# Kernel tuning notes

Hardware: AMD Instinct MI355X
Metric: run time of the kernel (lower is better)

The kernel has to match this reference:

```python
import jax, jax.numpy as jnp
import numpy as np

VOCAB, D, H = 30522, 768, 128
B, S = 32, 1024
N_SENT, SENT_LEN = 16, 64


def _lstm_dir(x, W_ih, W_hh, b, reverse=False):
    """Single-direction LSTM, PyTorch gate order (i,f,g,o). x: [B,T,D] -> [B,T,H]."""
    pre = jnp.einsum('btd,gd->btg', x, W_ih) + b  # [B,T,4H]
    if reverse:
        pre = pre[:, ::-1]
    nb = x.shape[0]
    h0 = jnp.zeros((nb, H), x.dtype)

    def step(carry, xt):
        h, c = carry
        g = xt + h @ W_hh.T
        i, f, gg, o = jnp.split(g, 4, axis=-1)
        c = jax.nn.sigmoid(f) * c + jax.nn.sigmoid(i) * jnp.tanh(gg)
        h = jax.nn.sigmoid(o) * jnp.tanh(c)
        return (h, c), h

    _, hs = jax.lax.scan(step, (h0, h0), jnp.swapaxes(pre, 0, 1))
    hs = jnp.swapaxes(hs, 0, 1)  # [B,T,H]
    if reverse:
        hs = hs[:, ::-1]
    return hs


def _bilstm(x, Wf, Uf, bf, Wb, Ub, bb):
    return jnp.concatenate([_lstm_dir(x, Wf, Uf, bf, False),
                            _lstm_dir(x, Wb, Ub, bb, True)], axis=-1)


def setup_inputs() -> dict:
    key = jax.random.key(0)
    ks = jax.random.split(key, 20)
    p = lambda i, shape: (jax.random.normal(ks[i], shape, dtype=jnp.float32) * 0.05)
    inp = {
        'word_inputs': jax.random.randint(ks[0], (B, S), 0, VOCAB, dtype=jnp.int32),
        'sent_tokens': jax.random.randint(ks[1], (B, N_SENT, SENT_LEN), 0, VOCAB, dtype=jnp.int32),
        'seq_len': S,
        'E': p(2, (VOCAB, D)),
        'lstm_Wih_f': p(3, (4 * H, D)), 'lstm_Whh_f': p(4, (4 * H, H)), 'lstm_b_f': p(5, (4 * H,)),
        'lstm_Wih_b': p(6, (4 * H, D)), 'lstm_Whh_b': p(7, (4 * H, H)), 'lstm_b_b': p(8, (4 * H,)),
        'sent_Wih_f': p(9, (4 * H, D)), 'sent_Whh_f': p(10, (4 * H, H)), 'sent_b_f': p(11, (4 * H,)),
        'sent_Wih_b': p(12, (4 * H, D)), 'sent_Whh_b': p(13, (4 * H, H)), 'sent_b_b': p(14, (4 * H,)),
        'gate_W': p(15, (2 * H, 4 * H)), 'gate_b': p(16, (2 * H,)),
    }
    return inp


def reference(word_inputs, sent_tokens, seq_len, E,
              lstm_Wih_f, lstm_Whh_f, lstm_b_f, lstm_Wih_b, lstm_Whh_b, lstm_b_b,
              sent_Wih_f, sent_Whh_f, sent_b_f, sent_Wih_b, sent_Whh_b, sent_b_b,
              gate_W, gate_b):
    # wordrep: embedding lookup (full-length sequences, all-ones masks)
    word_rep = E[word_inputs]  # [B,S,D]
    feature_out = _bilstm(word_rep, lstm_Wih_f, lstm_Whh_f, lstm_b_f,
                          lstm_Wih_b, lstm_Whh_b, lstm_b_b)  # [B,S,2H]

    # per-sentence BiLSTM: each sentence has its own fresh hidden state, so
    # the original python loop over sentences == batched BiLSTM over (B*N, L)
    st = sent_tokens.reshape(B * N_SENT, SENT_LEN)
    sent_rep = E[st]  # [B*N, L, D]
    sent_out = _bilstm(sent_rep, sent_Wih_f, sent_Whh_f, sent_b_f,
                       sent_Wih_b, sent_Whh_b, sent_b_b)  # [B*N, L, 2H]
    feature_out_sents = sent_out.reshape(B, N_SENT * SENT_LEN, 2 * H)  # [B,S,2H]

    gamma = jax.nn.sigmoid(
        jnp.concatenate([feature_out, feature_out_sents], axis=-1) @ gate_W.T + gate_b)
    return gamma * feature_out + (1.0 - gamma) * feature_out_sents
```

## Files before the change

### kernel.cpp

```cpp
#include <hip/hip_runtime.h>

typedef unsigned short u16;
typedef __attribute__((ext_vector_type(8))) short short8;
typedef __attribute__((ext_vector_type(4))) float f32x4;

__device__ __forceinline__ u16 f2b(float f){
    unsigned u = __builtin_bit_cast(unsigned, f);
    u += 0x7fffu + ((u >> 16) & 1u);
    return (u16)(u >> 16);
}
__device__ __forceinline__ float b2f(u16 s){
    unsigned u = ((unsigned)s) << 16;
    return __builtin_bit_cast(float, u);
}
__device__ __forceinline__ float sigm(float x){ return 1.f/(1.f + __expf(-x)); }
__device__ __forceinline__ float tanhf2(float x){
    float e = __expf(2.f * x);
    return 1.f - 2.f/(1.f + e);
}

__global__ __launch_bounds__(256) void cvt_bf16(const float* __restrict__ s,
                                                u16* __restrict__ d, int n4){
    int i = blockIdx.x*256 + threadIdx.x;
    if (i < n4){
        float4 v = ((const float4*)s)[i];
        ushort4 o;
        o.x = f2b(v.x); o.y = f2b(v.y); o.z = f2b(v.z); o.w = f2b(v.w);
        ((ushort4*)d)[i] = o;
    }
}

__global__ __launch_bounds__(192) void cvt_wih_perm(const float* __restrict__ s,
                                                    u16* __restrict__ d){
    int r = blockIdx.x;
    int j = threadIdx.x;
    int g = r >> 7, u = r & 127;
    int ro = u * 4 + g;
    float4 v = ((const float4*)(s + (size_t)r * 768))[j];
    ushort4 o;
    o.x = f2b(v.x); o.y = f2b(v.y); o.z = f2b(v.z); o.w = f2b(v.w);
    ((ushort4*)(d + (size_t)ro * 768))[j] = o;
}

__global__ __launch_bounds__(256) void cvt_whh_perm(const float* __restrict__ s,
                                                    u16* __restrict__ d){
    int idx = blockIdx.x*256 + threadIdx.x;
    if (idx >= 512*32) return;
    int r = idx >> 5, j = idx & 31;
    int g = r >> 7, u = r & 127;
    int ro = u * 4 + g;
    float4 v = ((const float4*)(s + (size_t)r * 128))[j];
    ushort4 o;
    o.x = f2b(v.x); o.y = f2b(v.y); o.z = f2b(v.z); o.w = f2b(v.w);
    ((ushort4*)(d + (size_t)ro * 128))[j] = o;
}

__global__ __launch_bounds__(256) void gemm_embed(
    const u16* __restrict__ E, const int* __restrict__ tok,
    const u16* __restrict__ Wt, const float* __restrict__ bf_,
    const float* __restrict__ bb_, u16* __restrict__ pre, int sentMode)
{
    __shared__ __align__(16) u16 Asm[128*32];
    __shared__ __align__(16) u16 Bsm[128*32];
    const int m0 = blockIdx.x * 128, n0 = blockIdx.y * 128;
    const int tid = threadIdx.x;
    const int ar = tid >> 2, ch = (tid & 3) * 8;
    const u16* ap0 = E + (size_t)tok[m0 + ar] * 768 + ch;
    const u16* ap1 = E + (size_t)tok[m0 + 64 + ar] * 768 + ch;
    const u16* bp0 = Wt + (size_t)(n0 + ar) * 768 + ch;
    const u16* bp1 = Wt + (size_t)(n0 + 64 + ar) * 768 + ch;
    const int lane = tid & 63, wave = tid >> 6;
    const int wm = (wave >> 1) * 64, wn = (wave & 1) * 64;
    const int qr = lane >> 4, lr = lane & 15;
    f32x4 acc[4][4] = {};
    for (int k0 = 0; k0 < 768; k0 += 32){
        __syncthreads();
        *(short8*)&Asm[ar*32 + ch]      = *(const short8*)(ap0 + k0);
        *(short8*)&Asm[(64+ar)*32 + ch] = *(const short8*)(ap1 + k0);
        *(short8*)&Bsm[ar*32 + ch]      = *(const short8*)(bp0 + k0);
        *(short8*)&Bsm[(64+ar)*32 + ch] = *(const short8*)(bp1 + k0);
        __syncthreads();
        short8 af[4], bfr[4];
        #pragma unroll
        for (int i = 0; i < 4; ++i){
            af[i]  = *(const short8*)&Asm[(wm + i*16 + lr)*32 + qr*8];
            bfr[i] = *(const short8*)&Bsm[(wn + i*16 + lr)*32 + qr*8];
        }
        #pragma unroll
        for (int i = 0; i < 4; ++i)
            #pragma unroll
            for (int j = 0; j < 4; ++j)
                acc[i][j] = __builtin_amdgcn_mfma_f32_16x16x32_bf16(af[i], bfr[j], acc[i][j], 0, 0, 0);
    }
    #pragma unroll
    for (int j = 0; j < 4; ++j){
        int col = n0 + wn + j*16 + lr;
        int dirO = col >> 9, pcol = col & 511;
        int uu = pcol >> 2, gg = pcol & 3;
        float bias = (dirO ? bb_ : bf_)[gg*128 + uu];
        int wL = uu >> 4, uL = uu & 15;
        #pragma unroll
        for (int i = 0; i < 4; ++i){
            #pragma unroll
            for (int r = 0; r < 4; ++r){
                int mrow = m0 + wm + i*16 + qr*4 + r;
                int blk, t, cL, Tdim;
                if (sentMode){ int s = mrow >> 6;  t = mrow & 63;   blk = (dirO<<7) + (s >> 2); cL = s & 3; Tdim = 64; }
                else         { int b = mrow >> 10; t = mrow & 1023; blk = (dirO<<3) + (b >> 2); cL = b & 3; Tdim = 1024; }
                size_t idx = (((size_t)blk * Tdim + t) * 512 + (wL*64 + cL*16 + uL)) * 4 + gg;
                pre[idx] = f2b(acc[i][j][r] + bias);
            }
        }
    }
}

__global__ __launch_bounds__(512)
__attribute__((amdgpu_waves_per_eu(2)))
void lstm_rec(
    const u16* __restrict__ preW, const u16* __restrict__ preS,
    const u16* __restrict__ Whp,
    float* __restrict__ fo, float* __restrict__ fs)
{
    const int bg = blockIdx.x;
    const u16* preBlk; const u16* wh; float* out;
    int T, dir, grpb;
    if (bg < 16){
        dir = bg >> 3; grpb = bg & 7; T = 1024;
        preBlk = preW + (size_t)bg * 1024 * 2048;
        wh = Whp + (size_t)dir*512*128; out = fo;
    } else {
        int sg = bg - 16; dir = sg >> 7; grpb = sg & 127; T = 64;
        preBlk = preS + (size_t)sg * 64 * 2048;
        wh = Whp + (size_t)(2+dir)*512*128; out = fs;
    }
    const int tid  = threadIdx.x;
    const int w    = tid >> 6, lane = tid & 63;
    const int lr = lane & 15, qr = lane >> 4;
    const int t0 = dir ? (T-1) : 0;
    const int dt = dir ? -1 : 1;

    short8 aw[4][4];
    #pragma unroll
    for (int i = 0; i < 4; ++i)
        #pragma unroll
        for (int kk = 0; kk < 4; ++kk)
            asm volatile("global_load_dwordx4 %0, %1, off"
                         : "=v"(aw[i][kk])
                         : "v"(wh + (size_t)(w*64 + i*16 + lr)*128 + kk*32 + qr*8));
    asm volatile("s_waitcnt vmcnt(0)");
    __builtin_amdgcn_sched_barrier(0);

    __shared__ __align__(16) u16    hb[2][2048];
    __shared__ __align__(16) float4 rd[512];
    for (int k = tid; k < 4096; k += 512) ((u16*)hb)[k] = 0;

    const int cL = lane >> 4;
    const int ur = lane & 15;
    const int u  = w*16 + ur;
    const int chainG = grpb*4 + cL;
    float* po = out + ((size_t)chainG*T + t0)*256 + dir*128 + u;
    const long ostep = (long)dt * 256;

    const long pstep = (long)dt * 2048;
    const u16* p = preBlk + (long)t0 * 2048 + tid*4;
    ushort4 buf[4];
    buf[0] = *(const ushort4*)p;
    buf[1] = *(const ushort4*)(p + pstep);
    buf[2] = *(const ushort4*)(p + 2*pstep);
    p += 3*pstep;

    const int rdW0 = w*64 + lr*16;
    const int rdR  = w*64 + cL*16 + (ur ^ (cL<<2));
    const int hbW  = cL*128 + (u ^ (cL<<3));

    float cst = 0.f;
    __syncthreads();

#define LSTM_STEP(J, LOADJ) do {                                              \
    short8 bfr[4];                                                            \
    _Pragma("unroll")                                                         \
    for (int kk = 0; kk < 4; ++kk)                                            \
        bfr[kk] = *(const short8*)&hb[(J)&1][lr*128 + ((((kk)*4+qr) ^ lr)<<3)];\
    buf[LOADJ] = *(const ushort4*)p;                                          \
    p += pstep;                                                               \
    f32x4 acc[4] = {};                                                        \
    _Pragma("unroll")                                                         \
    for (int i = 0; i < 4; ++i)                                               \
        _Pragma("unroll")                                                     \
        for (int kk = 0; kk < 4; ++kk)                                        \
            acc[i] = __builtin_amdgcn_mfma_f32_16x16x32_bf16(aw[i][kk], bfr[kk], acc[i], 0, 0, 0); \
    if (lr < 4){                                                              \
        _Pragma("unroll")                                                     \
        for (int i = 0; i < 4; ++i)                                           \
            rd[rdW0 + ((i*4+qr) ^ (lr<<2))] = __builtin_bit_cast(float4, acc[i]); \
    }                                                                         \
    float4 g4 = rd[rdR];                                                      \
    ushort4 pc = buf[J];                                                      \
    float a0 = b2f(pc.x) + g4.x, a1 = b2f(pc.y) + g4.y;                       \
    float a2 = b2f(pc.z) + g4.z, a3 = b2f(pc.w) + g4.w;                       \
    float gi = sigm(a0), gf = sigm(a1);                                       \
    float gg = tanhf2(a2), go = sigm(a3);                                     \
    float c = gf*cst + gi*gg; cst = c;                                        \
    float h = go*tanhf2(c);                                                   \
    po[0] = h;                                                                \
    po += ostep;                                                              \
    hb[((J)&1)^1][hbW] = f2b(h);                                              \
    __builtin_amdgcn_sched_barrier(0);                                        \
    asm volatile("s_waitcnt lgkmcnt(0)");                                     \
    __builtin_amdgcn_s_barrier();                                             \
    __builtin_amdgcn_sched_barrier(0);                                        \
} while(0)

    for (int itBase = 0; itBase < T; itBase += 4){
        LSTM_STEP(0, 3);
        LSTM_STEP(1, 0);
        LSTM_STEP(2, 1);
        LSTM_STEP(3, 2);
    }
#undef LSTM_STEP
}

__global__ __launch_bounds__(256) void gemm_gate(
    const u16* __restrict__ gW, const float* __restrict__ gb,
    const float* __restrict__ fo, const float* __restrict__ fs,
    float* __restrict__ out)
{
    __shared__ __align__(16) u16 Asm[128*32];
    __shared__ __align__(16) u16 Bsm[128*32];
    const int m0 = blockIdx.x * 128, n0 = blockIdx.y * 128;
    const int tid = threadIdx.x;
    const int ar = tid >> 2, ch = (tid & 3) * 8;
    const float* af0 = fo + (size_t)(m0 + ar) * 256 + ch;
    const float* af1 = fo + (size_t)(m0 + 64 + ar) * 256 + ch;
    const float* as0 = fs + (size_t)(m0 + ar) * 256 + ch;
    const float* as1 = fs + (size_t)(m0 + 64 + ar) * 256 + ch;
    const u16* bp0 = gW + (size_t)(n0 + ar) * 512 + ch;
    const u16* bp1 = gW + (size_t)(n0 + 64 + ar) * 512 + ch;
    const int lane = tid & 63, wave = tid >> 6;
    const int wm = (wave >> 1) * 64, wn = (wave & 1) * 64;
    const int qr = lane >> 4, lr = lane & 15;
    f32x4 acc[4][4] = {};
    for (int k0 = 0; k0 < 512; k0 += 32){
        __syncthreads();
        const float* s0 = (k0 < 256) ? (af0 + k0) : (as0 + (k0 - 256));
        const float* s1 = (k0 < 256) ? (af1 + k0) : (as1 + (k0 - 256));
        float4 x0 = ((const float4*)s0)[0], x1 = ((const float4*)s0)[1];
        float4 y0 = ((const float4*)s1)[0], y1 = ((const float4*)s1)[1];
        ushort4 a0; a0.x=f2b(x0.x); a0.y=f2b(x0.y); a0.z=f2b(x0.z); a0.w=f2b(x0.w);
        ushort4 a1; a1.x=f2b(x1.x); a1.y=f2b(x1.y); a1.z=f2b(x1.z); a1.w=f2b(x1.w);
        ushort4 b0; b0.x=f2b(y0.x); b0.y=f2b(y0.y); b0.z=f2b(y0.z); b0.w=f2b(y0.w);
        ushort4 b1; b1.x=f2b(y1.x); b1.y=f2b(y1.y); b1.z=f2b(y1.z); b1.w=f2b(y1.w);
        *(ushort4*)&Asm[ar*32 + ch]          = a0;
        *(ushort4*)&Asm[ar*32 + ch + 4]      = a1;
        *(ushort4*)&Asm[(64+ar)*32 + ch]     = b0;
        *(ushort4*)&Asm[(64+ar)*32 + ch + 4] = b1;
        *(short8*)&Bsm[ar*32 + ch]      = *(const short8*)(bp0 + k0);
        *(short8*)&Bsm[(64+ar)*32 + ch] = *(const short8*)(bp1 + k0);
        __syncthreads();
        short8 af[4], bfr[4];
        #pragma unroll
        for (int i = 0; i < 4; ++i){
            af[i]  = *(const short8*)&Asm[(wm + i*16 + lr)*32 + qr*8];
            bfr[i] = *(const short8*)&Bsm[(wn + i*16 + lr)*32 + qr*8];
        }
        #pragma unroll
        for (int i = 0; i < 4; ++i)
            #pragma unroll
            for (int j = 0; j < 4; ++j)
                acc[i][j] = __builtin_amdgcn_mfma_f32_16x16x32_bf16(af[i], bfr[j], acc[i][j], 0, 0, 0);
    }
    #pragma unroll
    for (int j = 0; j < 4; ++j){
        int col = n0 + wn + j*16 + lr;
        float bias = gb[col];
        #pragma unroll
        for (int i = 0; i < 4; ++i){
            #pragma unroll
            for (int r = 0; r < 4; ++r){
                int row = m0 + wm + i*16 + qr*4 + r;
                size_t o = (size_t)row*256 + col;
                float gamma = sigm(acc[i][j][r] + bias);
                out[o] = gamma * fo[o] + (1.f - gamma) * fs[o];
            }
        }
    }
}

extern "C" void kernel_launch(void* const* d_in, const int* in_sizes, int n_in,
                              void* d_out, int out_size, void* d_ws, size_t ws_size,
                              hipStream_t stream)
{
    (void)in_sizes; (void)n_in; (void)out_size; (void)ws_size;
    const int*   wordTok = (const int*)d_in[0];
    const int*   sentTok = (const int*)d_in[1];
    const float* E       = (const float*)d_in[3];
    const float* WihWf   = (const float*)d_in[4];
    const float* WhhWf   = (const float*)d_in[5];
    const float* bWf     = (const float*)d_in[6];
    const float* WihWb   = (const float*)d_in[7];
    const float* WhhWb   = (const float*)d_in[8];
    const float* bWb     = (const float*)d_in[9];
    const float* WihSf   = (const float*)d_in[10];
    const float* WhhSf   = (const float*)d_in[11];
    const float* bSf     = (const float*)d_in[12];
    const float* WihSb   = (const float*)d_in[13];
    const float* WhhSb   = (const float*)d_in[14];
    const float* bSb     = (const float*)d_in[15];
    const float* gateW   = (const float*)d_in[16];
    const float* gateB   = (const float*)d_in[17];
    float* out = (float*)d_out;

    char* w = (char*)d_ws;
    u16* Eb   = (u16*)w;  w += (size_t)30522*768*2;
    u16* Ww   = (u16*)w;  w += (size_t)1024*768*2;
    u16* Ws_  = (u16*)w;  w += (size_t)1024*768*2;
    u16* gWb  = (u16*)w;  w += (size_t)256*512*2;
    u16* preW = (u16*)w;  w += (size_t)32768*1024*2;
    u16* preS = (u16*)w;  w += (size_t)32768*1024*2;
    float* fo = (float*)w; w += (size_t)32768*256*4;
    float* fs = (float*)w; w += (size_t)32768*256*4;
    u16* Whp  = (u16*)w;  w += (size_t)4*512*128*2;

    const int nE4 = 30522*768/4;
    cvt_bf16<<<(nE4+255)/256, 256, 0, stream>>>(E, Eb, nE4);
    cvt_wih_perm<<<512, 192, 0, stream>>>(WihWf, Ww);
    cvt_wih_perm<<<512, 192, 0, stream>>>(WihWb, Ww + 512*768);
    cvt_wih_perm<<<512, 192, 0, stream>>>(WihSf, Ws_);
    cvt_wih_perm<<<512, 192, 0, stream>>>(WihSb, Ws_ + 512*768);
    const int nG4 = 256*512/4;
    cvt_bf16<<<(nG4+255)/256, 256, 0, stream>>>(gateW, gWb, nG4);
    cvt_whh_perm<<<64, 256, 0, stream>>>(WhhWf, Whp);
    cvt_whh_perm<<<64, 256, 0, stream>>>(WhhWb, Whp + 512*128);
    cvt_whh_perm<<<64, 256, 0, stream>>>(WhhSf, Whp + 2*512*128);
    cvt_whh_perm<<<64, 256, 0, stream>>>(WhhSb, Whp + 3*512*128);

    gemm_embed<<<dim3(256,8), 256, 0, stream>>>(Eb, wordTok, Ww, bWf, bWb, preW, 0);
    gemm_embed<<<dim3(256,8), 256, 0, stream>>>(Eb, sentTok, Ws_, bSf, bSb, preS, 1);
    lstm_rec<<<272, 512, 0, stream>>>(preW, preS, Whp, fo, fs);
    gemm_gate<<<dim3(256,2), 256, 0, stream>>>(gWb, gateB, fo, fs, out);
}
```

Before: 1.132 ms.

## Stage LSTM hidden outputs in LDS ring and flush coalesced float4 stores

Rather than writing each step's scalar h straight to global memory, hidden outputs go into a 16-step LDS history ring and are flushed every 8 steps as coalesced float4 stores. The hidden-state buffer is also shrunk so that only the lanes holding real chains (lr<4) read it, with a different XOR swizzle and the other MFMA B rows left zero. The aim is to cut scattered global stores on the serial recurrence path, at the cost of extra LDS and a periodic flush. The flush reads ring slots that later steps overwrite, and it relies on the barriers between steps for correctness.

```diff
diff --git a/kernel.cpp b/kernel.cpp
--- a/kernel.cpp
+++ b/kernel.cpp
@@ -150,16 +150,14 @@
     asm volatile("s_waitcnt vmcnt(0)");
     __builtin_amdgcn_sched_barrier(0);
 
-    __shared__ __align__(16) u16    hb[2][2048];
+    __shared__ __align__(16) u16    hb[2][512];
     __shared__ __align__(16) float4 rd[512];
-    for (int k = tid; k < 4096; k += 512) ((u16*)hb)[k] = 0;
+    __shared__ __align__(16) float  hist[16*512];
+    for (int k = tid; k < 1024; k += 512) ((u16*)hb)[k] = 0;
 
     const int cL = lane >> 4;
     const int ur = lane & 15;
     const int u  = w*16 + ur;
-    const int chainG = grpb*4 + cL;
-    float* po = out + ((size_t)chainG*T + t0)*256 + dir*128 + u;
-    const long ostep = (long)dt * 256;
 
     const long pstep = (long)dt * 2048;
     const u16* p = preBlk + (long)t0 * 2048 + tid*4;
@@ -171,16 +169,19 @@
 
     const int rdW0 = w*64 + lr*16;
     const int rdR  = w*64 + cL*16 + (ur ^ (cL<<2));
-    const int hbW  = cL*128 + (u ^ (cL<<3));
+    const int hbW  = cL*128 + (u ^ (cL<<4));
+    const int rxor = lr << 4;
 
     float cst = 0.f;
+    short8 bfr[4] = {};
     __syncthreads();
 
 #define LSTM_STEP(J, LOADJ) do {                                              \
-    short8 bfr[4];                                                            \
-    _Pragma("unroll")                                                         \
-    for (int kk = 0; kk < 4; ++kk)                                            \
-        bfr[kk] = *(const short8*)&hb[(J)&1][lr*128 + ((((kk)*4+qr) ^ lr)<<3)];\
+    if (lr < 4){                                                              \
+        _Pragma("unroll")                                                     \
+        for (int kk = 0; kk < 4; ++kk)                                        \
+            bfr[kk] = *(const short8*)&hb[(J)&1][lr*128 + ((((kk)*4+qr)<<3) ^ rxor)]; \
+    }                                                                         \
     buf[LOADJ] = *(const ushort4*)p;                                          \
     p += pstep;                                                               \
     f32x4 acc[4] = {};                                                        \
@@ -202,8 +203,7 @@
     float gg = tanhf2(a2), go = sigm(a3);                                     \
     float c = gf*cst + gi*gg; cst = c;                                        \
     float h = go*tanhf2(c);                                                   \
-    po[0] = h;                                                                \
-    po += ostep;                                                              \
+    hist[(ib15 + (J))*512 + tid] = h;                                         \
     hb[((J)&1)^1][hbW] = f2b(h);                                              \
     __builtin_amdgcn_sched_barrier(0);                                        \
     asm volatile("s_waitcnt lgkmcnt(0)");                                     \
@@ -212,10 +212,27 @@
 } while(0)
 
     for (int itBase = 0; itBase < T; itBase += 4){
+        const int ib15 = itBase & 15;
         LSTM_STEP(0, 3);
         LSTM_STEP(1, 0);
         LSTM_STEP(2, 1);
         LSTM_STEP(3, 2);
+        if ((itBase & 7) == 4){
+            const int fBase = itBase - 4;
+            const int fb = fBase & 15;
+            #pragma unroll
+            for (int j2 = 0; j2 < 2; ++j2){
+                int lin  = j2*512 + tid;
+                int s    = lin >> 7;
+                int quad = lin & 127;
+                int wq = quad >> 4;
+                int cq = (quad >> 2) & 3;
+                int uq = (quad & 3) * 4;
+                float4 v = *(const float4*)&hist[((fb + s) & 15)*512 + quad*4];
+                int tt = t0 + dt*(fBase + s);
+                *(float4*)(out + ((size_t)(grpb*4 + cq)*T + tt)*256 + dir*128 + wq*16 + uq) = v;
+            }
+        }
     }
 #undef LSTM_STEP
 }
```

Measured after the change: 1.152 ms. No clear change (+1.8%).

## Remove LDS reduction round-trip in LSTM recurrence via register gate selection

Applied to the files above, without the earlier changes.

Changes the thread-to-unit mapping in the recurrent kernel so each lane picks its gate values straight out of the MFMA accumulators with selects, instead of writing results to shared memory and reading them back. The hidden-state buffer shrinks to a compact layout with a new XOR swizzle, and the precompute GEMM's output permutation changes to match the new per-thread ordering. This removes one LDS write/read pair per timestep from the serial critical path, in exchange for extra select instructions and a tighter coupling between the two kernels' layouts.

```diff
diff --git a/kernel.cpp b/kernel.cpp
--- a/kernel.cpp
+++ b/kernel.cpp
@@ -99,6 +99,7 @@
         int uu = pcol >> 2, gg = pcol & 3;
         float bias = (dirO ? bb_ : bf_)[gg*128 + uu];
         int wL = uu >> 4, uL = uu & 15;
+        int tidPart = wL*64 + (uL & 3)*16 + (uL & 12);
         #pragma unroll
         for (int i = 0; i < 4; ++i){
             #pragma unroll
@@ -107,7 +108,7 @@
                 int blk, t, cL, Tdim;
                 if (sentMode){ int s = mrow >> 6;  t = mrow & 63;   blk = (dirO<<7) + (s >> 2); cL = s & 3; Tdim = 64; }
                 else         { int b = mrow >> 10; t = mrow & 1023; blk = (dirO<<3) + (b >> 2); cL = b & 3; Tdim = 1024; }
-                size_t idx = (((size_t)blk * Tdim + t) * 512 + (wL*64 + cL*16 + uL)) * 4 + gg;
+                size_t idx = (((size_t)blk * Tdim + t) * 512 + (tidPart + cL)) * 4 + gg;
                 pre[idx] = f2b(acc[i][j][r] + bias);
             }
         }
@@ -150,13 +151,16 @@
     asm volatile("s_waitcnt vmcnt(0)");
     __builtin_amdgcn_sched_barrier(0);
 
-    __shared__ __align__(16) u16    hb[2][2048];
-    __shared__ __align__(16) float4 rd[512];
-    for (int k = tid; k < 4096; k += 512) ((u16*)hb)[k] = 0;
-
-    const int cL = lane >> 4;
-    const int ur = lane & 15;
-    const int u  = w*16 + ur;
+    __shared__ __align__(16) u16 hb[2][512];
+    for (int k = tid; k < 1024; k += 512) ((u16*)hb)[k] = 0;
+
+    const int cL = lr & 3;
+    const int u  = w*16 + (lr >> 2)*4 + qr;
+    const int hbW   = cL*128 + (u ^ (cL << 4));
+    const int rbase = cL*128;
+    const int rxor  = cL << 4;
+    const bool s2 = (lr & 4) != 0, s3 = (lr & 8) != 0;
+
     const int chainG = grpb*4 + cL;
     float* po = out + ((size_t)chainG*T + t0)*256 + dir*128 + u;
     const long ostep = (long)dt * 256;
@@ -169,10 +173,6 @@
     buf[2] = *(const ushort4*)(p + 2*pstep);
     p += 3*pstep;
 
-    const int rdW0 = w*64 + lr*16;
-    const int rdR  = w*64 + cL*16 + (ur ^ (cL<<2));
-    const int hbW  = cL*128 + (u ^ (cL<<3));
-
     float cst = 0.f;
     __syncthreads();
 
@@ -180,26 +180,26 @@
     short8 bfr[4];                                                            \
     _Pragma("unroll")                                                         \
     for (int kk = 0; kk < 4; ++kk)                                            \
-        bfr[kk] = *(const short8*)&hb[(J)&1][lr*128 + ((((kk)*4+qr) ^ lr)<<3)];\
+        bfr[kk] = *(const short8*)&hb[(J)&1][rbase + ((kk*32 + qr*8) ^ rxor)];\
     buf[LOADJ] = *(const ushort4*)p;                                          \
     p += pstep;                                                               \
-    f32x4 acc[4] = {};                                                        \
+    f32x4 a0 = {}, a1 = {}, a2 = {}, a3 = {};                                 \
     _Pragma("unroll")                                                         \
-    for (int i = 0; i < 4; ++i)                                               \
-        _Pragma("unroll")                                                     \
-        for (int kk = 0; kk < 4; ++kk)                                        \
-            acc[i] = __builtin_amdgcn_mfma_f32_16x16x32_bf16(aw[i][kk], bfr[kk], acc[i], 0, 0, 0); \
-    if (lr < 4){                                                              \
-        _Pragma("unroll")                                                     \
-        for (int i = 0; i < 4; ++i)                                           \
-            rd[rdW0 + ((i*4+qr) ^ (lr<<2))] = __builtin_bit_cast(float4, acc[i]); \
+    for (int kk = 0; kk < 4; ++kk){                                           \
+        a0 = __builtin_amdgcn_mfma_f32_16x16x32_bf16(aw[0][kk], bfr[kk], a0, 0, 0, 0); \
+        a1 = __builtin_amdgcn_mfma_f32_16x16x32_bf16(aw[1][kk], bfr[kk], a1, 0, 0, 0); \
+        a2 = __builtin_amdgcn_mfma_f32_16x16x32_bf16(aw[2][kk], bfr[kk], a2, 0, 0, 0); \
+        a3 = __builtin_amdgcn_mfma_f32_16x16x32_bf16(aw[3][kk], bfr[kk], a3, 0, 0, 0); \
     }                                                                         \
-    float4 g4 = rd[rdR];                                                      \
+    float m0 = s3 ? (s2 ? a3[0] : a2[0]) : (s2 ? a1[0] : a0[0]);              \
+    float m1 = s3 ? (s2 ? a3[1] : a2[1]) : (s2 ? a1[1] : a0[1]);              \
+    float m2 = s3 ? (s2 ? a3[2] : a2[2]) : (s2 ? a1[2] : a0[2]);              \
+    float m3 = s3 ? (s2 ? a3[3] : a2[3]) : (s2 ? a1[3] : a0[3]);              \
     ushort4 pc = buf[J];                                                      \
-    float a0 = b2f(pc.x) + g4.x, a1 = b2f(pc.y) + g4.y;                       \
-    float a2 = b2f(pc.z) + g4.z, a3 = b2f(pc.w) + g4.w;                       \
-    float gi = sigm(a0), gf = sigm(a1);                                       \
-    float gg = tanhf2(a2), go = sigm(a3);                                     \
+    float g0 = b2f(pc.x) + m0, g1 = b2f(pc.y) + m1;                           \
+    float g2 = b2f(pc.z) + m2, g3 = b2f(pc.w) + m3;                           \
+    float gi = sigm(g0), gf = sigm(g1);                                       \
+    float gg = tanhf2(g2), go = sigm(g3);                                     \
     float c = gf*cst + gi*gg; cst = c;                                        \
     float h = go*tanhf2(c);                                                   \
     po[0] = h;                                                                \
```

Result: faster. 1.095 ms (-3.3%).
